# Kernel tuning notes

Hardware: AMD Instinct MI355X
Metric: run time of the kernel (lower is better)

## Reference

```python
import jax, jax.numpy as jnp
import numpy as np

BLOCKSIZE = 64
# Fixed NF4 codebook (bitsandbytes normal-float 4-bit quantiles)
NF4_CODE = jnp.array([
    -1.0, -0.6961928009986877, -0.5250730514526367, -0.39491748809814453,
    -0.28444138169288635, -0.18477343022823334, -0.09105003625154495, 0.0,
    0.07958029955625534, 0.16093020141124725, 0.24611230194568634,
    0.33791524171829224, 0.44070982933044434, 0.5626170039176941,
    0.7229568362236023, 1.0], dtype=jnp.float32)


def setup_inputs() -> dict:
    key = jax.random.key(0)
    k1, k2, k3, k4 = jax.random.split(key, 4)
    B, IN, OUT = 32, 4096, 14336
    x = jax.random.normal(k1, (B, IN), dtype=jnp.float32)
    codes = jax.random.randint(k2, (OUT, IN), 0, 16, dtype=jnp.int32)
    absmax = jax.random.uniform(k3, (OUT * IN // BLOCKSIZE,), dtype=jnp.float32)
    bias = jax.random.normal(k4, (OUT,), dtype=jnp.float32)
    return {"x": x, "codes": codes, "absmax": absmax, "bias": bias}


def reference(x, codes, absmax, bias):
    out_f, in_f = codes.shape
    # Dequantize: codebook lookup then per-block (64) absmax scaling
    w = NF4_CODE[codes].reshape(-1, BLOCKSIZE) * absmax[:, None]  # [nblocks, 64]
    w = w.reshape(out_f, in_f)
    # y = x @ W^T + bias  (matmul_4bit semantics)
    return jnp.einsum('bi,oi->bo', x, w) + bias
```

## Files before the change

### kernel.cpp

```cpp
#include <hip/hip_runtime.h>
#include <stddef.h>
#include <stdint.h>

#define B_   32
#define IN_  4096
#define OUT_ 14336

typedef short v8s __attribute__((ext_vector_type(8)));
typedef float v4f __attribute__((ext_vector_type(4)));

__device__ __constant__ float c_nf4[16] = {
    -1.0f, -0.6961928009986877f, -0.5250730514526367f, -0.39491748809814453f,
    -0.28444138169288635f, -0.18477343022823334f, -0.09105003625154495f, 0.0f,
    0.07958029955625534f, 0.16093020141124725f, 0.24611230194568634f,
    0.33791524171829224f, 0.44070982933044434f, 0.5626170039176941f,
    0.7229568362236023f, 1.0f};

__device__ __forceinline__ unsigned f2bf_u(float f) {
    union { float f; unsigned u; } v; v.f = f;
    return (v.u + 0x7FFFu + ((v.u >> 16) & 1u)) >> 16;
}
__device__ __forceinline__ unsigned pack2(float lo, float hi) {
    return f2bf_u(lo) | (f2bf_u(hi) << 16);
}

__global__ __launch_bounds__(256) void prep(const float* __restrict__ x,
                                            unsigned* __restrict__ xB) {
    int t  = blockIdx.x * 256 + threadIdx.x;
    int kt = t >> 7;
    int bt = (t >> 6) & 1;
    int l  = t & 63;
    int b  = bt * 16 + (l & 15);
    int k0 = kt * 32 + (l >> 4) * 8;
    const float* xr = x + (size_t)b * IN_ + k0;
    float4 a = *(const float4*)xr;
    float4 c = *(const float4*)(xr + 4);
    uint4 w;
    w.x = pack2(a.x, a.y);
    w.y = pack2(a.z, a.w);
    w.z = pack2(c.x, c.y);
    w.w = pack2(c.z, c.w);
    *(uint4*)(xB + (size_t)t * 4) = w;
}

__global__ __launch_bounds__(256) void init_out(const float* __restrict__ bias,
                                                float* __restrict__ out) {
    int t   = blockIdx.x * 256 + threadIdx.x;
    int o   = (t * 4) % OUT_;
    int row = (t * 4) / OUT_;
    float4 bv = *(const float4*)(bias + o);
    *(float4*)(out + (size_t)row * OUT_ + o) = bv;
}

__global__ __launch_bounds__(256) void nf4_mfma(
    const int* __restrict__ codes, const float* __restrict__ absmax,
    const unsigned* __restrict__ xB, float* __restrict__ out) {
    __shared__ unsigned plut[256];
    plut[threadIdx.x] = pack2(c_nf4[threadIdx.x & 15], c_nf4[threadIdx.x >> 4]);
    __syncthreads();

    const int w  = threadIdx.x >> 6;
    const int l  = threadIdx.x & 63;
    const int o0 = blockIdx.x * 64 + w * 16;
    const int kq = blockIdx.y;
    const int m  = l & 15;
    const int q  = l >> 4;

    const int kt0 = kq * 32;
    const int*   crow = codes + (size_t)(o0 + m) * IN_ + q * 8 + (size_t)kt0 * 32;
    const uint4* xbp  = (const uint4*)xB + l + (size_t)kt0 * 128;
    const float* amp  = absmax + (size_t)(o0 + q * 4) * 64 + kq * 16;

    v4f main0 = {0.f, 0.f, 0.f, 0.f};
    v4f main1 = {0.f, 0.f, 0.f, 0.f};
    const v4f zro = {0.f, 0.f, 0.f, 0.f};

#pragma unroll 2
    for (int kb = 0; kb < 16; ++kb) {
        const int* cA = crow + (size_t)kb * 64;
        int4 c0 = *(const int4*)(cA);
        int4 c1 = *(const int4*)(cA + 4);
        int4 c2 = *(const int4*)(cA + 32);
        int4 c3 = *(const int4*)(cA + 36);
        uint4 b0 = xbp[(size_t)kb * 256];
        uint4 b1 = xbp[(size_t)kb * 256 + 64];
        uint4 b2 = xbp[(size_t)kb * 256 + 128];
        uint4 b3 = xbp[(size_t)kb * 256 + 192];
        float am0 = amp[kb];
        float am1 = amp[kb + 64];
        float am2 = amp[kb + 128];
        float am3 = amp[kb + 192];

        union { uint4 u; v8s v; } aA, aB, f0, f1, f2, f3;
        aA.u.x = plut[c0.x | (c0.y << 4)];
        aA.u.y = plut[c0.z | (c0.w << 4)];
        aA.u.z = plut[c1.x | (c1.y << 4)];
        aA.u.w = plut[c1.z | (c1.w << 4)];
        aB.u.x = plut[c2.x | (c2.y << 4)];
        aB.u.y = plut[c2.z | (c2.w << 4)];
        aB.u.z = plut[c3.x | (c3.y << 4)];
        aB.u.w = plut[c3.z | (c3.w << 4)];
        f0.u = b0; f1.u = b1; f2.u = b2; f3.u = b3;

        v4f blk0 = __builtin_amdgcn_mfma_f32_16x16x32_bf16(aA.v, f0.v, zro, 0, 0, 0);
        v4f blk1 = __builtin_amdgcn_mfma_f32_16x16x32_bf16(aA.v, f1.v, zro, 0, 0, 0);
        blk0 = __builtin_amdgcn_mfma_f32_16x16x32_bf16(aB.v, f2.v, blk0, 0, 0, 0);
        blk1 = __builtin_amdgcn_mfma_f32_16x16x32_bf16(aB.v, f3.v, blk1, 0, 0, 0);

        main0[0] += am0 * blk0[0];  main1[0] += am0 * blk1[0];
        main0[1] += am1 * blk0[1];  main1[1] += am1 * blk1[1];
        main0[2] += am2 * blk0[2];  main1[2] += am2 * blk1[2];
        main0[3] += am3 * blk0[3];  main1[3] += am3 * blk1[3];
    }

    const int bc = l & 15;
    const int ob = o0 + q * 4;
#pragma unroll
    for (int r = 0; r < 4; ++r) {
        atomicAdd(&out[(size_t)bc * OUT_ + ob + r],        main0[r]);
        atomicAdd(&out[(size_t)(bc + 16) * OUT_ + ob + r], main1[r]);
    }
}

extern "C" void kernel_launch(void* const* d_in, const int* in_sizes, int n_in,
                              void* d_out, int out_size, void* d_ws, size_t ws_size,
                              hipStream_t stream) {
    const float* x      = (const float*)d_in[0];
    const int*   codes  = (const int*)d_in[1];
    const float* absmax = (const float*)d_in[2];
    const float* bias   = (const float*)d_in[3];
    float* out = (float*)d_out;
    unsigned* xB = (unsigned*)d_ws;

    init_out<<<dim3(448), 256, 0, stream>>>(bias, out);
    prep<<<dim3(64), 256, 0, stream>>>(x, xB);
    nf4_mfma<<<dim3(OUT_ / 64, 4), 256, 0, stream>>>(codes, absmax, xB, out);
}
```

Before: 335.6 us.

## Pre-pack int32 NF4 codes into nibbles before the MFMA GEMV

Adds a pack_codes kernel that reads the int32 codes once with nontemporal loads, packs eight 4-bit codes per word and writes them in an order matching the MFMA lane layout. The main kernel then loads one uint4 of packed codes per two k-blocks instead of four int4 loads per block, and indexes the LDS LUT with byte extracts. The full 235MB int32 read still happens each call, now in a separate streaming kernel, plus a 29MB write and re-read of the packed buffer. The benefit depends on the pack pass streaming better than the original strided gather.

```diff
diff --git a/kernel.cpp b/kernel.cpp
--- a/kernel.cpp
+++ b/kernel.cpp
@@ -8,6 +8,7 @@
 
 typedef short v8s __attribute__((ext_vector_type(8)));
 typedef float v4f __attribute__((ext_vector_type(4)));
+typedef int   v4i __attribute__((ext_vector_type(4)));
 
 __device__ __constant__ float c_nf4[16] = {
     -1.0f, -0.6961928009986877f, -0.5250730514526367f, -0.39491748809814453f,
@@ -52,8 +53,28 @@
     *(float4*)(out + (size_t)row * OUT_ + o) = bv;
 }
 
+__global__ __launch_bounds__(256) void pack_codes(const int* __restrict__ codes,
+                                                  unsigned* __restrict__ pk) {
+    const size_t total = (size_t)OUT_ * 512;
+    size_t t = (size_t)blockIdx.x * 256 + threadIdx.x;
+    for (; t < total; t += (size_t)gridDim.x * 256) {
+        const v4i* src = (const v4i*)(codes + t * 8);
+        v4i a = __builtin_nontemporal_load(src);
+        v4i b = __builtin_nontemporal_load(src + 1);
+        unsigned d = (unsigned)(a.x & 15)        | ((unsigned)(a.y & 15) << 4)  |
+                     ((unsigned)(a.z & 15) << 8)  | ((unsigned)(a.w & 15) << 12) |
+                     ((unsigned)(b.x & 15) << 16) | ((unsigned)(b.y & 15) << 20) |
+                     ((unsigned)(b.z & 15) << 24) | ((unsigned)(b.w & 15) << 28);
+        unsigned K8 = (unsigned)(t & 511);
+        unsigned kq = K8 >> 7, r = K8 & 127;
+        unsigned kb = r >> 3, s = (r >> 2) & 1, q = r & 3;
+        unsigned pidx = kq * 128 + (kb >> 1) * 16 + q * 4 + (kb & 1) * 2 + s;
+        pk[(t & ~(size_t)511) + pidx] = d;
+    }
+}
+
 __global__ __launch_bounds__(256) void nf4_mfma(
-    const int* __restrict__ codes, const float* __restrict__ absmax,
+    const unsigned* __restrict__ pk, const float* __restrict__ absmax,
     const unsigned* __restrict__ xB, float* __restrict__ out) {
     __shared__ unsigned plut[256];
     plut[threadIdx.x] = pack2(c_nf4[threadIdx.x & 15], c_nf4[threadIdx.x >> 4]);
@@ -66,51 +87,64 @@
     const int m  = l & 15;
     const int q  = l >> 4;
 
-    const int kt0 = kq * 32;
-    const int*   crow = codes + (size_t)(o0 + m) * IN_ + q * 8 + (size_t)kt0 * 32;
-    const uint4* xbp  = (const uint4*)xB + l + (size_t)kt0 * 128;
-    const float* amp  = absmax + (size_t)(o0 + q * 4) * 64 + kq * 16;
+    const unsigned* prow = pk + (size_t)(o0 + m) * 512 + kq * 128 + q * 4;
+    const uint4*    xbp  = (const uint4*)xB + l + (size_t)(kq * 32) * 128;
+    const float*    amp  = absmax + (size_t)(o0 + q * 4) * 64 + kq * 16;
 
     v4f main0 = {0.f, 0.f, 0.f, 0.f};
     v4f main1 = {0.f, 0.f, 0.f, 0.f};
     const v4f zro = {0.f, 0.f, 0.f, 0.f};
 
 #pragma unroll 2
-    for (int kb = 0; kb < 16; ++kb) {
-        const int* cA = crow + (size_t)kb * 64;
-        int4 c0 = *(const int4*)(cA);
-        int4 c1 = *(const int4*)(cA + 4);
-        int4 c2 = *(const int4*)(cA + 32);
-        int4 c3 = *(const int4*)(cA + 36);
-        uint4 b0 = xbp[(size_t)kb * 256];
-        uint4 b1 = xbp[(size_t)kb * 256 + 64];
-        uint4 b2 = xbp[(size_t)kb * 256 + 128];
-        uint4 b3 = xbp[(size_t)kb * 256 + 192];
-        float am0 = amp[kb];
-        float am1 = amp[kb + 64];
-        float am2 = amp[kb + 128];
-        float am3 = amp[kb + 192];
+    for (int kbp = 0; kbp < 8; ++kbp) {
+        uint4 pkv = *(const uint4*)(prow + kbp * 16);
+        const int kb0 = kbp * 2, kb1 = kbp * 2 + 1;
+        uint4 b0 = xbp[(size_t)kb0 * 256];
+        uint4 b1 = xbp[(size_t)kb0 * 256 + 64];
+        uint4 b2 = xbp[(size_t)kb0 * 256 + 128];
+        uint4 b3 = xbp[(size_t)kb0 * 256 + 192];
+        uint4 b4 = xbp[(size_t)kb1 * 256];
+        uint4 b5 = xbp[(size_t)kb1 * 256 + 64];
+        uint4 b6 = xbp[(size_t)kb1 * 256 + 128];
+        uint4 b7 = xbp[(size_t)kb1 * 256 + 192];
+        float am00 = amp[kb0],       am01 = amp[kb0 + 64];
+        float am02 = amp[kb0 + 128], am03 = amp[kb0 + 192];
+        float am10 = amp[kb1],       am11 = amp[kb1 + 64];
+        float am12 = amp[kb1 + 128], am13 = amp[kb1 + 192];
 
         union { uint4 u; v8s v; } aA, aB, f0, f1, f2, f3;
-        aA.u.x = plut[c0.x | (c0.y << 4)];
-        aA.u.y = plut[c0.z | (c0.w << 4)];
-        aA.u.z = plut[c1.x | (c1.y << 4)];
-        aA.u.w = plut[c1.z | (c1.w << 4)];
-        aB.u.x = plut[c2.x | (c2.y << 4)];
-        aB.u.y = plut[c2.z | (c2.w << 4)];
-        aB.u.z = plut[c3.x | (c3.y << 4)];
-        aB.u.w = plut[c3.z | (c3.w << 4)];
+
+        aA.u.x = plut[pkv.x & 0xff];         aA.u.y = plut[(pkv.x >> 8) & 0xff];
+        aA.u.z = plut[(pkv.x >> 16) & 0xff]; aA.u.w = plut[pkv.x >> 24];
+        aB.u.x = plut[pkv.y & 0xff];         aB.u.y = plut[(pkv.y >> 8) & 0xff];
+        aB.u.z = plut[(pkv.y >> 16) & 0xff]; aB.u.w = plut[pkv.y >> 24];
         f0.u = b0; f1.u = b1; f2.u = b2; f3.u = b3;
+        {
+            v4f blk0 = __builtin_amdgcn_mfma_f32_16x16x32_bf16(aA.v, f0.v, zro, 0, 0, 0);
+            v4f blk1 = __builtin_amdgcn_mfma_f32_16x16x32_bf16(aA.v, f1.v, zro, 0, 0, 0);
+            blk0 = __builtin_amdgcn_mfma_f32_16x16x32_bf16(aB.v, f2.v, blk0, 0, 0, 0);
+            blk1 = __builtin_amdgcn_mfma_f32_16x16x32_bf16(aB.v, f3.v, blk1, 0, 0, 0);
+            main0[0] += am00 * blk0[0];  main1[0] += am00 * blk1[0];
+            main0[1] += am01 * blk0[1];  main1[1] += am01 * blk1[1];
+            main0[2] += am02 * blk0[2];  main1[2] += am02 * blk1[2];
+            main0[3] += am03 * blk0[3];  main1[3] += am03 * blk1[3];
+        }
 
-        v4f blk0 = __builtin_amdgcn_mfma_f32_16x16x32_bf16(aA.v, f0.v, zro, 0, 0, 0);
-        v4f blk1 = __builtin_amdgcn_mfma_f32_16x16x32_bf16(aA.v, f1.v, zro, 0, 0, 0);
-        blk0 = __builtin_amdgcn_mfma_f32_16x16x32_bf16(aB.v, f2.v, blk0, 0, 0, 0);
-        blk1 = __builtin_amdgcn_mfma_f32_16x16x32_bf16(aB.v, f3.v, blk1, 0, 0, 0);
-
-        main0[0] += am0 * blk0[0];  main1[0] += am0 * blk1[0];
-        main0[1] += am1 * blk0[1];  main1[1] += am1 * blk1[1];
-        main0[2] += am2 * blk0[2];  main1[2] += am2 * blk1[2];
-        main0[3] += am3 * blk0[3];  main1[3] += am3 * blk1[3];
+        aA.u.x = plut[pkv.z & 0xff];         aA.u.y = plut[(pkv.z >> 8) & 0xff];
+        aA.u.z = plut[(pkv.z >> 16) & 0xff]; aA.u.w = plut[pkv.z >> 24];
+        aB.u.x = plut[pkv.w & 0xff];         aB.u.y = plut[(pkv.w >> 8) & 0xff];
+        aB.u.z = plut[(pkv.w >> 16) & 0xff]; aB.u.w = plut[pkv.w >> 24];
+        f0.u = b4; f1.u = b5; f2.u = b6; f3.u = b7;
+        {
+            v4f blk0 = __builtin_amdgcn_mfma_f32_16x16x32_bf16(aA.v, f0.v, zro, 0, 0, 0);
+            v4f blk1 = __builtin_amdgcn_mfma_f32_16x16x32_bf16(aA.v, f1.v, zro, 0, 0, 0);
+            blk0 = __builtin_amdgcn_mfma_f32_16x16x32_bf16(aB.v, f2.v, blk0, 0, 0, 0);
+            blk1 = __builtin_amdgcn_mfma_f32_16x16x32_bf16(aB.v, f3.v, blk1, 0, 0, 0);
+            main0[0] += am10 * blk0[0];  main1[0] += am10 * blk1[0];
+            main0[1] += am11 * blk0[1];  main1[1] += am11 * blk1[1];
+            main0[2] += am12 * blk0[2];  main1[2] += am12 * blk1[2];
+            main0[3] += am13 * blk0[3];  main1[3] += am13 * blk1[3];
+        }
     }
 
     const int bc = l & 15;
@@ -131,8 +165,10 @@
     const float* bias   = (const float*)d_in[3];
     float* out = (float*)d_out;
     unsigned* xB = (unsigned*)d_ws;
+    unsigned* pk = (unsigned*)((char*)d_ws + (1u << 20));
 
+    pack_codes<<<dim3(2048), 256, 0, stream>>>(codes, pk);
     init_out<<<dim3(448), 256, 0, stream>>>(bias, out);
     prep<<<dim3(64), 256, 0, stream>>>(x, xB);
-    nf4_mfma<<<dim3(OUT_ / 64, 4), 256, 0, stream>>>(codes, absmax, xB, out);
+    nf4_mfma<<<dim3(OUT_ / 64, 4), 256, 0, stream>>>(pk, absmax, xB, out);
 }
```

Result: slower. 354.2 us (+5.5%).

## Replace split-K atomics with in-block LDS reduction and fuse bias init

Applied to the files above, without the earlier changes.

Restructures the GEMV so each 512-thread block covers 32 output rows, with the four K-quarters handled by different waves in the same block. Partial sums are reduced through shared memory and written once with bias added, which removes the init_out launch and all global atomicAdds. Code loads become nontemporal to avoid polluting cache with the streamed weights. The cost is fewer, larger blocks, an extra barrier, and more LDS use per block.

```diff
diff --git a/kernel.cpp b/kernel.cpp
--- a/kernel.cpp
+++ b/kernel.cpp
@@ -8,6 +8,7 @@
 
 typedef short v8s __attribute__((ext_vector_type(8)));
 typedef float v4f __attribute__((ext_vector_type(4)));
+typedef int   v4i __attribute__((ext_vector_type(4)));
 
 __device__ __constant__ float c_nf4[16] = {
     -1.0f, -0.6961928009986877f, -0.5250730514526367f, -0.39491748809814453f,
@@ -43,45 +44,38 @@
     *(uint4*)(xB + (size_t)t * 4) = w;
 }
 
-__global__ __launch_bounds__(256) void init_out(const float* __restrict__ bias,
-                                                float* __restrict__ out) {
-    int t   = blockIdx.x * 256 + threadIdx.x;
-    int o   = (t * 4) % OUT_;
-    int row = (t * 4) / OUT_;
-    float4 bv = *(const float4*)(bias + o);
-    *(float4*)(out + (size_t)row * OUT_ + o) = bv;
-}
-
-__global__ __launch_bounds__(256) void nf4_mfma(
+__global__ __launch_bounds__(512, 4) void nf4_mfma(
     const int* __restrict__ codes, const float* __restrict__ absmax,
-    const unsigned* __restrict__ xB, float* __restrict__ out) {
+    const unsigned* __restrict__ xB, const float* __restrict__ bias,
+    float* __restrict__ out) {
     __shared__ unsigned plut[256];
-    plut[threadIdx.x] = pack2(c_nf4[threadIdx.x & 15], c_nf4[threadIdx.x >> 4]);
+    __shared__ float red[4][32][33];
+    if (threadIdx.x < 256)
+        plut[threadIdx.x] = pack2(c_nf4[threadIdx.x & 15], c_nf4[threadIdx.x >> 4]);
     __syncthreads();
 
     const int w  = threadIdx.x >> 6;
     const int l  = threadIdx.x & 63;
-    const int o0 = blockIdx.x * 64 + w * 16;
-    const int kq = blockIdx.y;
+    const int ot = w & 1;
+    const int ks = w >> 1;
+    const int o0 = blockIdx.x * 32 + ot * 16;
     const int m  = l & 15;
     const int q  = l >> 4;
 
-    const int kt0 = kq * 32;
-    const int*   crow = codes + (size_t)(o0 + m) * IN_ + q * 8 + (size_t)kt0 * 32;
-    const uint4* xbp  = (const uint4*)xB + l + (size_t)kt0 * 128;
-    const float* amp  = absmax + (size_t)(o0 + q * 4) * 64 + kq * 16;
+    const int*   crow = codes + (size_t)(o0 + m) * IN_ + (size_t)ks * 1024 + q * 8;
+    const uint4* xbp  = (const uint4*)xB + l + (size_t)(ks * 32) * 128;
+    const float* amp  = absmax + (size_t)(o0 + q * 4) * 64 + ks * 16;
 
     v4f main0 = {0.f, 0.f, 0.f, 0.f};
     v4f main1 = {0.f, 0.f, 0.f, 0.f};
     const v4f zro = {0.f, 0.f, 0.f, 0.f};
 
-#pragma unroll 2
     for (int kb = 0; kb < 16; ++kb) {
-        const int* cA = crow + (size_t)kb * 64;
-        int4 c0 = *(const int4*)(cA);
-        int4 c1 = *(const int4*)(cA + 4);
-        int4 c2 = *(const int4*)(cA + 32);
-        int4 c3 = *(const int4*)(cA + 36);
+        const int* cA = crow + kb * 64;
+        v4i c0 = __builtin_nontemporal_load((const v4i*)(cA));
+        v4i c1 = __builtin_nontemporal_load((const v4i*)(cA + 4));
+        v4i c2 = __builtin_nontemporal_load((const v4i*)(cA + 32));
+        v4i c3 = __builtin_nontemporal_load((const v4i*)(cA + 36));
         uint4 b0 = xbp[(size_t)kb * 256];
         uint4 b1 = xbp[(size_t)kb * 256 + 64];
         uint4 b2 = xbp[(size_t)kb * 256 + 128];
@@ -113,13 +107,23 @@
         main0[3] += am3 * blk0[3];  main1[3] += am3 * blk1[3];
     }
 
-    const int bc = l & 15;
-    const int ob = o0 + q * 4;
+    const int rr = ot * 16 + q * 4;
 #pragma unroll
     for (int r = 0; r < 4; ++r) {
-        atomicAdd(&out[(size_t)bc * OUT_ + ob + r],        main0[r]);
-        atomicAdd(&out[(size_t)(bc + 16) * OUT_ + ob + r], main1[r]);
+        red[ks][rr + r][m]      = main0[r];
+        red[ks][rr + r][m + 16] = main1[r];
     }
+    __syncthreads();
+
+    const int c  = threadIdx.x >> 4;
+    const int r2 = (threadIdx.x & 15) * 2;
+    const int o  = blockIdx.x * 32 + r2;
+    float s0 = red[0][r2][c] + red[1][r2][c] + red[2][r2][c] + red[3][r2][c]
+             + bias[o];
+    float s1 = red[0][r2 + 1][c] + red[1][r2 + 1][c] + red[2][r2 + 1][c]
+             + red[3][r2 + 1][c] + bias[o + 1];
+    float2 st = {s0, s1};
+    *(float2*)(out + (size_t)c * OUT_ + o) = st;
 }
 
 extern "C" void kernel_launch(void* const* d_in, const int* in_sizes, int n_in,
@@ -132,7 +136,6 @@
     float* out = (float*)d_out;
     unsigned* xB = (unsigned*)d_ws;
 
-    init_out<<<dim3(448), 256, 0, stream>>>(bias, out);
     prep<<<dim3(64), 256, 0, stream>>>(x, xB);
-    nf4_mfma<<<dim3(OUT_ / 64, 4), 256, 0, stream>>>(codes, absmax, xB, out);
+    nf4_mfma<<<dim3(OUT_ / 32), 512, 0, stream>>>(codes, absmax, xB, bias, out);
 }
```

Measured after the change: 337.0 us. No clear change (+0.4%).

## Drop split-K and atomics, fuse bias into store, use nontemporal code loads

Applied to the files above, without the earlier changes.

Removes the 4-way K split so each block handles the full reduction of 64 output rows, and writes results directly with the bias added instead of running a separate bias-init kernel followed by atomic adds. The codes stream is read with nontemporal loads so it does not pollute the cache. This saves one launch and the atomic traffic, but cuts the grid from 896 blocks to 224, which may underfill the GPU and leave less parallelism for hiding memory latency on the bandwidth-bound codes stream.

```diff
diff --git a/kernel.cpp b/kernel.cpp
--- a/kernel.cpp
+++ b/kernel.cpp
@@ -8,6 +8,7 @@
 
 typedef short v8s __attribute__((ext_vector_type(8)));
 typedef float v4f __attribute__((ext_vector_type(4)));
+typedef int   v4i __attribute__((ext_vector_type(4)));
 
 __device__ __constant__ float c_nf4[16] = {
     -1.0f, -0.6961928009986877f, -0.5250730514526367f, -0.39491748809814453f,
@@ -43,18 +44,10 @@
     *(uint4*)(xB + (size_t)t * 4) = w;
 }
 
-__global__ __launch_bounds__(256) void init_out(const float* __restrict__ bias,
-                                                float* __restrict__ out) {
-    int t   = blockIdx.x * 256 + threadIdx.x;
-    int o   = (t * 4) % OUT_;
-    int row = (t * 4) / OUT_;
-    float4 bv = *(const float4*)(bias + o);
-    *(float4*)(out + (size_t)row * OUT_ + o) = bv;
-}
-
 __global__ __launch_bounds__(256) void nf4_mfma(
     const int* __restrict__ codes, const float* __restrict__ absmax,
-    const unsigned* __restrict__ xB, float* __restrict__ out) {
+    const unsigned* __restrict__ xB, const float* __restrict__ bias,
+    float* __restrict__ out) {
     __shared__ unsigned plut[256];
     plut[threadIdx.x] = pack2(c_nf4[threadIdx.x & 15], c_nf4[threadIdx.x >> 4]);
     __syncthreads();
@@ -62,26 +55,24 @@
     const int w  = threadIdx.x >> 6;
     const int l  = threadIdx.x & 63;
     const int o0 = blockIdx.x * 64 + w * 16;
-    const int kq = blockIdx.y;
     const int m  = l & 15;
     const int q  = l >> 4;
 
-    const int kt0 = kq * 32;
-    const int*   crow = codes + (size_t)(o0 + m) * IN_ + q * 8 + (size_t)kt0 * 32;
-    const uint4* xbp  = (const uint4*)xB + l + (size_t)kt0 * 128;
-    const float* amp  = absmax + (size_t)(o0 + q * 4) * 64 + kq * 16;
+    const int*   crow = codes + (size_t)(o0 + m) * IN_ + q * 8;
+    const uint4* xbp  = (const uint4*)xB + l;
+    const float* amp  = absmax + (size_t)(o0 + q * 4) * 64;
 
     v4f main0 = {0.f, 0.f, 0.f, 0.f};
     v4f main1 = {0.f, 0.f, 0.f, 0.f};
     const v4f zro = {0.f, 0.f, 0.f, 0.f};
 
 #pragma unroll 2
-    for (int kb = 0; kb < 16; ++kb) {
+    for (int kb = 0; kb < 64; ++kb) {
         const int* cA = crow + (size_t)kb * 64;
-        int4 c0 = *(const int4*)(cA);
-        int4 c1 = *(const int4*)(cA + 4);
-        int4 c2 = *(const int4*)(cA + 32);
-        int4 c3 = *(const int4*)(cA + 36);
+        v4i c0 = __builtin_nontemporal_load((const v4i*)(cA));
+        v4i c1 = __builtin_nontemporal_load((const v4i*)(cA + 4));
+        v4i c2 = __builtin_nontemporal_load((const v4i*)(cA + 32));
+        v4i c3 = __builtin_nontemporal_load((const v4i*)(cA + 36));
         uint4 b0 = xbp[(size_t)kb * 256];
         uint4 b1 = xbp[(size_t)kb * 256 + 64];
         uint4 b2 = xbp[(size_t)kb * 256 + 128];
@@ -117,8 +108,9 @@
     const int ob = o0 + q * 4;
 #pragma unroll
     for (int r = 0; r < 4; ++r) {
-        atomicAdd(&out[(size_t)bc * OUT_ + ob + r],        main0[r]);
-        atomicAdd(&out[(size_t)(bc + 16) * OUT_ + ob + r], main1[r]);
+        float bv = bias[ob + r];
+        out[(size_t)bc * OUT_ + ob + r]        = main0[r] + bv;
+        out[(size_t)(bc + 16) * OUT_ + ob + r] = main1[r] + bv;
     }
 }
 
@@ -132,7 +124,6 @@
     float* out = (float*)d_out;
     unsigned* xB = (unsigned*)d_ws;
 
-    init_out<<<dim3(448), 256, 0, stream>>>(bias, out);
     prep<<<dim3(64), 256, 0, stream>>>(x, xB);
-    nf4_mfma<<<dim3(OUT_ / 64, 4), 256, 0, stream>>>(codes, absmax, xB, out);
+    nf4_mfma<<<dim3(OUT_ / 64), 256, 0, stream>>>(codes, absmax, xB, bias, out);
 }
```

After: 333.7 us. About the same (-0.6%).
